# Kernel tuning notes

Measured on AMD Instinct MI355X. Metric: run time of the kernel, lower is better.

Reference implementation:

```python
import jax, jax.numpy as jnp
import numpy as np

TEMPERATURE = 0.07
BASE_TEMPERATURE = 0.07
N_CLASSES = 100


def setup_inputs() -> dict:
    key = jax.random.key(0)
    k1, k2, k3 = jax.random.split(key, 3)
    B, V, D = 4096, 2, 512
    features = jax.random.normal(k1, (B, V, D), dtype=jnp.float32)
    labels = jax.random.randint(k2, (B,), 0, N_CLASSES, dtype=jnp.int64)
    global_protos = jax.random.normal(k3, (N_CLASSES, D), dtype=jnp.float32)
    return {"features": features, "labels": labels, "global_protos": global_protos}


def reference(features, labels, global_protos):
    B, V, D = features.shape
    # contrast_feature = cat(unbind(features, dim=1)) -> view-major ordering [V*B, D]
    contrast = jnp.transpose(features, (1, 0, 2)).reshape(V * B, D)
    # anchor rows are prototypes gathered by label, tiled over views (contrast_mode='all')
    anchor = jnp.tile(global_protos[labels], (V, 1))          # [V*B, D]
    logits = (anchor @ contrast.T) / TEMPERATURE              # [V*B, V*B]
    logits = logits - jax.lax.stop_gradient(jnp.max(logits, axis=1, keepdims=True))
    # positive mask from label equality, tiled; diagonal (self-contrast) removed
    pos = (labels[:, None] == labels[None, :]).astype(jnp.float32)  # [B, B]
    mask = jnp.tile(pos, (V, V))                               # [V*B, V*B]
    logits_mask = 1.0 - jnp.eye(V * B, dtype=jnp.float32)
    mask = mask * logits_mask
    exp_logits = jnp.exp(logits) * logits_mask
    log_prob = logits - jnp.log(jnp.sum(exp_logits, axis=1, keepdims=True))
    mean_log_prob_pos = jnp.sum(mask * log_prob, axis=1) / jnp.sum(mask, axis=1)
    loss = -(TEMPERATURE / BASE_TEMPERATURE) * mean_log_prob_pos
    return jnp.mean(loss.reshape(V, B))
```

## Files before the change

kernel.cpp:

```cpp
#include <hip/hip_runtime.h>
#include <hip/hip_bf16.h>
#include <math.h>

#define BS 4096
#define DD 512
#define NCLS 100
#define NROWS 8192
#define NSLAB 256
#define INV_T (1.0f / 0.07f)

typedef __attribute__((ext_vector_type(8))) short short8;
typedef __attribute__((ext_vector_type(4))) float f32x4;

__device__ __forceinline__ unsigned short f2bf(float x) {
    __hip_bfloat16 h = __float2bfloat16(x);
    return *reinterpret_cast<unsigned short*>(&h);
}

__global__ __launch_bounds__(512) void k_gemm(const float* __restrict__ feats,
                                              const float* __restrict__ protos,
                                              const int* __restrict__ labels,
                                              float4* __restrict__ PA,
                                              float4* __restrict__ PB,
                                              float* __restrict__ stash,
                                              float* __restrict__ out) {
    __shared__ char lds[32 * DD * 2];
    const int nt = blockIdx.x, tid = threadIdx.x;
    if (nt == 0 && tid == 0) out[0] = 0.f;
    const int v  = nt >> 7;
    const int b0 = (nt & 127) * 32;

    float4 fr[8];
#pragma unroll
    for (int it = 0; it < 8; ++it) {
        const int i = tid + it * 512;
        const int r = i >> 7, c4 = i & 127;
        fr[it] = *(const float4*)(feats + (size_t)((b0 + r) * 2 + v) * DD + c4 * 4);
    }
#pragma unroll
    for (int it = 0; it < 8; ++it) {
        const int i = tid + it * 512;
        const int r = i >> 7, c4 = i & 127;
        ushort4 o = { f2bf(fr[it].x), f2bf(fr[it].y), f2bf(fr[it].z), f2bf(fr[it].w) };
        const int byte = (r * 1024 + c4 * 8) ^ ((r & 7) << 4);
        *reinterpret_cast<ushort4*>(&lds[byte]) = o;
    }
    __syncthreads();

    const int w = tid >> 6, lane = tid & 63;
    const int m = lane & 15, kb = lane >> 4;
    const int arow = min(w * 16 + m, NCLS - 1);
    const float4* ap = (const float4*)(protos + (size_t)arow * DD + kb * 8);

    const int swz   = (m & 7) << 4;
    const int base0 = m * 1024 + kb * 16;
    const int base1 = (m + 16) * 1024 + kb * 16;
    f32x4 acc0 = {}, acc1 = {};
#pragma unroll
    for (int k = 0; k < 16; ++k) {
        const float4 lo = ap[k * 8];
        const float4 hi = ap[k * 8 + 1];
        short8 a;
        a[0]=f2bf(lo.x); a[1]=f2bf(lo.y); a[2]=f2bf(lo.z); a[3]=f2bf(lo.w);
        a[4]=f2bf(hi.x); a[5]=f2bf(hi.y); a[6]=f2bf(hi.z); a[7]=f2bf(hi.w);
        const short8 bf0 = *reinterpret_cast<const short8*>(&lds[(base0 + k * 64) ^ swz]);
        const short8 bf1 = *reinterpret_cast<const short8*>(&lds[(base1 + k * 64) ^ swz]);
        acc0 = __builtin_amdgcn_mfma_f32_16x16x32_bf16(a, bf0, acc0, 0, 0, 0);
        acc1 = __builtin_amdgcn_mfma_f32_16x16x32_bf16(a, bf1, acc1, 0, 0, 0);
    }
#pragma unroll
    for (int r = 0; r < 4; ++r) { acc0[r] *= INV_T; acc1[r] *= INV_T; }

    const int j0 = nt * 32 + m, j1 = j0 + 16;
    const int lb0 = labels[j0 & (BS - 1)], lb1 = labels[j1 & (BS - 1)];

    if ((lb0 >> 4) == w && ((lb0 >> 2) & 3) == kb) {
        const int rr = lb0 & 3;
        stash[j0] = (rr==0)?acc0[0]:(rr==1)?acc0[1]:(rr==2)?acc0[2]:acc0[3];
    }
    if ((lb1 >> 4) == w && ((lb1 >> 2) & 3) == kb) {
        const int rr = lb1 & 3;
        stash[j1] = (rr==0)?acc1[0]:(rr==1)?acc1[1]:(rr==2)?acc1[2]:acc1[3];
    }

#pragma unroll
    for (int r = 0; r < 4; ++r) {
        const int row = w * 16 + kb * 4 + r;
        const float x0 = acc0[r], x1 = acc1[r];
        float m1, m2; int i1;
        if (x0 >= x1) { m1 = x0; m2 = x1; i1 = j0; } else { m1 = x1; m2 = x0; i1 = j1; }
#pragma unroll
        for (int s = 1; s < 16; s <<= 1) {
            const float om1 = __shfl_xor(m1, s);
            const float om2 = __shfl_xor(m2, s);
            const int   oi1 = __shfl_xor(i1, s);
            if (om1 > m1) { m2 = fmaxf(m1, om2); m1 = om1; i1 = oi1; }
            else          { m2 = fmaxf(m2, om1); }
        }
        float ea = __expf(x0 - m1) + __expf(x1 - m1);
        float ee = (j0 != i1 ? __expf(x0 - m2) : 0.f) + (j1 != i1 ? __expf(x1 - m2) : 0.f);
        float pp = 0.f, nn = 0.f;
        if (lb0 == row) { pp += x0 - m1; nn += 1.f; }
        if (lb1 == row) { pp += x1 - m1; nn += 1.f; }
#pragma unroll
        for (int s = 1; s < 16; s <<= 1) {
            ea += __shfl_xor(ea, s);
            ee += __shfl_xor(ee, s);
            pp += __shfl_xor(pp, s);
            nn += __shfl_xor(nn, s);
        }
        if (m == 0 && row < NCLS) {
            PA[row * NSLAB + nt] = make_float4(m1, m2, ea, ee);
            PB[row * NSLAB + nt] = make_float4(pp, nn, (float)i1, 0.f);
        }
    }
}

__global__ __launch_bounds__(256) void k_merge(const float4* __restrict__ PA,
                                               const float4* __restrict__ PB,
                                               const float* __restrict__ stash,
                                               const int* __restrict__ labels,
                                               float* __restrict__ out) {
    const int c = blockIdx.x, tid = threadIdx.x;
    const float4 A  = PA[c * NSLAB + tid];
    const float4 Bq = PB[c * NSLAB + tid];
    const float m1 = A.x, m2 = A.y, ea = A.z, ee = A.w;
    const float pp = Bq.x, nn = Bq.y;
    const int   i1 = (int)Bq.z;

    __shared__ float s1[256], s2[256];
    __shared__ int   si[256];
    s1[tid] = m1; s2[tid] = m2; si[tid] = i1;
    __syncthreads();
    for (int s = 128; s > 0; s >>= 1) {
        if (tid < s) {
            const float b1 = s1[tid + s], b2 = s2[tid + s];
            if (b1 > s1[tid]) { s2[tid] = fmaxf(s1[tid], b2); s1[tid] = b1; si[tid] = si[tid + s]; }
            else              { s2[tid] = fmaxf(s2[tid], b1); }
        }
        __syncthreads();
    }
    const float gm1 = s1[0], gm2 = s2[0];
    const int   gi1 = si[0];
    __syncthreads();

    const float e1c = ea * __expf(m1 - gm1);
    const float e2c = ((gi1 >> 5) == tid) ? ee * __expf(m2 - gm2)
                                          : ea * __expf(m1 - gm2);
    const float pc  = pp + nn * (m1 - gm1);
    __shared__ float r1[256], r2[256], r3[256];
    r1[tid] = e1c; r2[tid] = e2c; r3[tid] = pc;
    __syncthreads();
    for (int s = 128; s > 0; s >>= 1) {
        if (tid < s) { r1[tid] += r1[tid + s]; r2[tid] += r2[tid + s]; r3[tid] += r3[tid + s]; }
        __syncthreads();
    }
    const float E1 = r1[0], E2 = r2[0], Pg = r3[0];
    __syncthreads();

    float ls = 0.f;
    const float tmax = (gm2 - gm1) + __logf(E2);
    for (int it = 0; it < 8; ++it) {
        const int j = it * 1024 + tid * 4;
        const int4   lv = *(const int4*)(labels + (j & (BS - 1)));
        const float4 sv = *(const float4*)(stash + j);
        if (lv.x == c) ls += (j + 0 == gi1) ? tmax : __logf(E1 - __expf(sv.x - gm1));
        if (lv.y == c) ls += (j + 1 == gi1) ? tmax : __logf(E1 - __expf(sv.y - gm1));
        if (lv.z == c) ls += (j + 2 == gi1) ? tmax : __logf(E1 - __expf(sv.z - gm1));
        if (lv.w == c) ls += (j + 3 == gi1) ? tmax : __logf(E1 - __expf(sv.w - gm1));
    }
    s1[tid] = ls;
    __syncthreads();
    for (int s = 128; s > 0; s >>= 1) {
        if (tid < s) s1[tid] += s1[tid + s];
        __syncthreads();
    }
    if (tid == 0) atomicAdd(out, (s1[0] - Pg) / (float)NROWS);
}

extern "C" void kernel_launch(void* const* d_in, const int* in_sizes, int n_in,
                              void* d_out, int out_size, void* d_ws, size_t ws_size,
                              hipStream_t stream) {
    const float* feats  = (const float*)d_in[0];
    const int*   labels = (const int*)d_in[1];
    const float* protos = (const float*)d_in[2];
    float* out = (float*)d_out;

    char* w = (char*)d_ws;
    size_t off = 0;
    auto take = [&](size_t n) { size_t o = off; off += (n + 255) & ~(size_t)255; return o; };
    float4* PA    = (float4*)(w + take((size_t)NCLS * NSLAB * 16));
    float4* PB    = (float4*)(w + take((size_t)NCLS * NSLAB * 16));
    float*  stash = (float*)(w + take((size_t)NROWS * 4));

    k_gemm<<<NSLAB, 512, 0, stream>>>(feats, protos, labels, PA, PB, stash, out);
    k_merge<<<NCLS, 256, 0, stream>>>(PA, PB, stash, labels, out);
}
```

Before: 83.80 us.

## Pre-convert prototypes to bf16 and halve per-block column tile to 16

Adds a prep kernel that converts the 100 prototype rows to bf16 once into workspace and zeroes the output. The GEMM kernel then loads bf16 A fragments directly instead of converting fp32 per block. Each block now covers 16 contrast columns instead of 32, so there are 512 blocks for more parallelism across CUs. The merge kernel widens to 512 threads to reduce the larger partial set. This costs an extra kernel launch and doubles the partial-statistics traffic.

Result: no change. 84.19 us (+0.5%).

```diff
diff --git a/kernel.cpp b/kernel.cpp
--- a/kernel.cpp
+++ b/kernel.cpp
@@ -6,10 +6,11 @@
 #define DD 512
 #define NCLS 100
 #define NROWS 8192
-#define NSLAB 256
+#define NSLAB 512
 #define INV_T (1.0f / 0.07f)
 
 typedef __attribute__((ext_vector_type(8))) short short8;
+typedef __attribute__((ext_vector_type(8))) unsigned short ushort8;
 typedef __attribute__((ext_vector_type(4))) float f32x4;
 
 __device__ __forceinline__ unsigned short f2bf(float x) {
@@ -17,28 +18,49 @@
     return *reinterpret_cast<unsigned short*>(&h);
 }
 
+__global__ __launch_bounds__(256) void k_prep(const float* __restrict__ protos,
+                                              unsigned short* __restrict__ pB,
+                                              float* __restrict__ out) {
+    const int bid = blockIdx.x, tid = threadIdx.x;
+    if (bid < 28) {
+        const int t = bid * 256 + tid;
+        const int r = t >> 6;
+        const int kk = (t & 63) << 3;
+        float4 f0 = {0,0,0,0}, f1 = {0,0,0,0};
+        if (r < NCLS) {
+            const float4* s = (const float4*)(protos + (size_t)r * DD + kk);
+            f0 = s[0]; f1 = s[1];
+        }
+        ushort8 o;
+        o[0]=f2bf(f0.x); o[1]=f2bf(f0.y); o[2]=f2bf(f0.z); o[3]=f2bf(f0.w);
+        o[4]=f2bf(f1.x); o[5]=f2bf(f1.y); o[6]=f2bf(f1.z); o[7]=f2bf(f1.w);
+        *reinterpret_cast<ushort8*>(pB + (size_t)r * DD + kk) = o;
+    } else if (tid == 0) {
+        out[0] = 0.f;
+    }
+}
+
 __global__ __launch_bounds__(512) void k_gemm(const float* __restrict__ feats,
-                                              const float* __restrict__ protos,
+                                              const unsigned short* __restrict__ pB,
                                               const int* __restrict__ labels,
                                               float4* __restrict__ PA,
-                                              float4* __restrict__ PB,
-                                              float* __restrict__ stash,
-                                              float* __restrict__ out) {
-    __shared__ char lds[32 * DD * 2];
+                                              float4* __restrict__ PBd,
+                                              float* __restrict__ stash)
+{
+    __shared__ char lds[16 * DD * 2];
     const int nt = blockIdx.x, tid = threadIdx.x;
-    if (nt == 0 && tid == 0) out[0] = 0.f;
-    const int v  = nt >> 7;
-    const int b0 = (nt & 127) * 32;
-
-    float4 fr[8];
-#pragma unroll
-    for (int it = 0; it < 8; ++it) {
+    const int v  = nt >> 8;
+    const int b0 = (nt & 255) * 16;
+
+    float4 fr[4];
+#pragma unroll
+    for (int it = 0; it < 4; ++it) {
         const int i = tid + it * 512;
         const int r = i >> 7, c4 = i & 127;
         fr[it] = *(const float4*)(feats + (size_t)((b0 + r) * 2 + v) * DD + c4 * 4);
     }
 #pragma unroll
-    for (int it = 0; it < 8; ++it) {
+    for (int it = 0; it < 4; ++it) {
         const int i = tid + it * 512;
         const int r = i >> 7, c4 = i & 127;
         ushort4 o = { f2bf(fr[it].x), f2bf(fr[it].y), f2bf(fr[it].z), f2bf(fr[it].w) };
@@ -50,45 +72,33 @@
     const int w = tid >> 6, lane = tid & 63;
     const int m = lane & 15, kb = lane >> 4;
     const int arow = min(w * 16 + m, NCLS - 1);
-    const float4* ap = (const float4*)(protos + (size_t)arow * DD + kb * 8);
-
-    const int swz   = (m & 7) << 4;
-    const int base0 = m * 1024 + kb * 16;
-    const int base1 = (m + 16) * 1024 + kb * 16;
-    f32x4 acc0 = {}, acc1 = {};
+    const short8* apv = (const short8*)((const short*)pB + (size_t)arow * DD + kb * 8);
+
+    const int swz  = (m & 7) << 4;
+    const int base = m * 1024 + kb * 16;
+    f32x4 acc = {};
 #pragma unroll
     for (int k = 0; k < 16; ++k) {
-        const float4 lo = ap[k * 8];
-        const float4 hi = ap[k * 8 + 1];
-        short8 a;
-        a[0]=f2bf(lo.x); a[1]=f2bf(lo.y); a[2]=f2bf(lo.z); a[3]=f2bf(lo.w);
-        a[4]=f2bf(hi.x); a[5]=f2bf(hi.y); a[6]=f2bf(hi.z); a[7]=f2bf(hi.w);
-        const short8 bf0 = *reinterpret_cast<const short8*>(&lds[(base0 + k * 64) ^ swz]);
-        const short8 bf1 = *reinterpret_cast<const short8*>(&lds[(base1 + k * 64) ^ swz]);
-        acc0 = __builtin_amdgcn_mfma_f32_16x16x32_bf16(a, bf0, acc0, 0, 0, 0);
-        acc1 = __builtin_amdgcn_mfma_f32_16x16x32_bf16(a, bf1, acc1, 0, 0, 0);
-    }
-#pragma unroll
-    for (int r = 0; r < 4; ++r) { acc0[r] *= INV_T; acc1[r] *= INV_T; }
-
-    const int j0 = nt * 32 + m, j1 = j0 + 16;
-    const int lb0 = labels[j0 & (BS - 1)], lb1 = labels[j1 & (BS - 1)];
+        const short8 a = apv[k * 4];
+        const short8 b = *reinterpret_cast<const short8*>(&lds[(base + k * 64) ^ swz]);
+        acc = __builtin_amdgcn_mfma_f32_16x16x32_bf16(a, b, acc, 0, 0, 0);
+    }
+#pragma unroll
+    for (int r = 0; r < 4; ++r) acc[r] *= INV_T;
+
+    const int j0  = nt * 16 + m;
+    const int lb0 = labels[j0 & (BS - 1)];
 
     if ((lb0 >> 4) == w && ((lb0 >> 2) & 3) == kb) {
         const int rr = lb0 & 3;
-        stash[j0] = (rr==0)?acc0[0]:(rr==1)?acc0[1]:(rr==2)?acc0[2]:acc0[3];
-    }
-    if ((lb1 >> 4) == w && ((lb1 >> 2) & 3) == kb) {
-        const int rr = lb1 & 3;
-        stash[j1] = (rr==0)?acc1[0]:(rr==1)?acc1[1]:(rr==2)?acc1[2]:acc1[3];
+        stash[j0] = (rr==0)?acc[0]:(rr==1)?acc[1]:(rr==2)?acc[2]:acc[3];
     }
 
 #pragma unroll
     for (int r = 0; r < 4; ++r) {
         const int row = w * 16 + kb * 4 + r;
-        const float x0 = acc0[r], x1 = acc1[r];
-        float m1, m2; int i1;
-        if (x0 >= x1) { m1 = x0; m2 = x1; i1 = j0; } else { m1 = x1; m2 = x0; i1 = j1; }
+        const float x0 = acc[r];
+        float m1 = x0, m2 = -INFINITY; int i1 = j0;
 #pragma unroll
         for (int s = 1; s < 16; s <<= 1) {
             const float om1 = __shfl_xor(m1, s);
@@ -97,11 +107,10 @@
             if (om1 > m1) { m2 = fmaxf(m1, om2); m1 = om1; i1 = oi1; }
             else          { m2 = fmaxf(m2, om1); }
         }
-        float ea = __expf(x0 - m1) + __expf(x1 - m1);
-        float ee = (j0 != i1 ? __expf(x0 - m2) : 0.f) + (j1 != i1 ? __expf(x1 - m2) : 0.f);
-        float pp = 0.f, nn = 0.f;
-        if (lb0 == row) { pp += x0 - m1; nn += 1.f; }
-        if (lb1 == row) { pp += x1 - m1; nn += 1.f; }
+        float ea = __expf(x0 - m1);
+        float ee = (j0 != i1) ? __expf(x0 - m2) : 0.f;
+        float pp = (lb0 == row) ? x0 - m1 : 0.f;
+        float nn = (lb0 == row) ? 1.f : 0.f;
 #pragma unroll
         for (int s = 1; s < 16; s <<= 1) {
             ea += __shfl_xor(ea, s);
@@ -110,29 +119,29 @@
             nn += __shfl_xor(nn, s);
         }
         if (m == 0 && row < NCLS) {
-            PA[row * NSLAB + nt] = make_float4(m1, m2, ea, ee);
-            PB[row * NSLAB + nt] = make_float4(pp, nn, (float)i1, 0.f);
-        }
-    }
-}
-
-__global__ __launch_bounds__(256) void k_merge(const float4* __restrict__ PA,
-                                               const float4* __restrict__ PB,
+            PA[row * NSLAB + nt]  = make_float4(m1, m2, ea, ee);
+            PBd[row * NSLAB + nt] = make_float4(pp, nn, (float)i1, 0.f);
+        }
+    }
+}
+
+__global__ __launch_bounds__(512) void k_merge(const float4* __restrict__ PA,
+                                               const float4* __restrict__ PBd,
                                                const float* __restrict__ stash,
                                                const int* __restrict__ labels,
                                                float* __restrict__ out) {
     const int c = blockIdx.x, tid = threadIdx.x;
     const float4 A  = PA[c * NSLAB + tid];
-    const float4 Bq = PB[c * NSLAB + tid];
+    const float4 Bq = PBd[c * NSLAB + tid];
     const float m1 = A.x, m2 = A.y, ea = A.z, ee = A.w;
     const float pp = Bq.x, nn = Bq.y;
     const int   i1 = (int)Bq.z;
 
-    __shared__ float s1[256], s2[256];
-    __shared__ int   si[256];
+    __shared__ float s1[512], s2[512];
+    __shared__ int   si[512];
     s1[tid] = m1; s2[tid] = m2; si[tid] = i1;
     __syncthreads();
-    for (int s = 128; s > 0; s >>= 1) {
+    for (int s = 256; s > 0; s >>= 1) {
         if (tid < s) {
             const float b1 = s1[tid + s], b2 = s2[tid + s];
             if (b1 > s1[tid]) { s2[tid] = fmaxf(s1[tid], b2); s1[tid] = b1; si[tid] = si[tid + s]; }
@@ -145,13 +154,13 @@
     __syncthreads();
 
     const float e1c = ea * __expf(m1 - gm1);
-    const float e2c = ((gi1 >> 5) == tid) ? ee * __expf(m2 - gm2)
+    const float e2c = ((gi1 >> 4) == tid) ? ee * __expf(m2 - gm2)
                                           : ea * __expf(m1 - gm2);
     const float pc  = pp + nn * (m1 - gm1);
-    __shared__ float r1[256], r2[256], r3[256];
+    __shared__ float r1[512], r2[512], r3[512];
     r1[tid] = e1c; r2[tid] = e2c; r3[tid] = pc;
     __syncthreads();
-    for (int s = 128; s > 0; s >>= 1) {
+    for (int s = 256; s > 0; s >>= 1) {
         if (tid < s) { r1[tid] += r1[tid + s]; r2[tid] += r2[tid + s]; r3[tid] += r3[tid + s]; }
         __syncthreads();
     }
@@ -160,8 +169,8 @@
 
     float ls = 0.f;
     const float tmax = (gm2 - gm1) + __logf(E2);
-    for (int it = 0; it < 8; ++it) {
-        const int j = it * 1024 + tid * 4;
+    for (int it = 0; it < 4; ++it) {
+        const int j = it * 2048 + tid * 4;
         const int4   lv = *(const int4*)(labels + (j & (BS - 1)));
         const float4 sv = *(const float4*)(stash + j);
         if (lv.x == c) ls += (j + 0 == gi1) ? tmax : __logf(E1 - __expf(sv.x - gm1));
@@ -171,7 +180,7 @@
     }
     s1[tid] = ls;
     __syncthreads();
-    for (int s = 128; s > 0; s >>= 1) {
+    for (int s = 256; s > 0; s >>= 1) {
         if (tid < s) s1[tid] += s1[tid + s];
         __syncthreads();
     }
@@ -189,10 +198,12 @@
     char* w = (char*)d_ws;
     size_t off = 0;
     auto take = [&](size_t n) { size_t o = off; off += (n + 255) & ~(size_t)255; return o; };
-    float4* PA    = (float4*)(w + take((size_t)NCLS * NSLAB * 16));
-    float4* PB    = (float4*)(w + take((size_t)NCLS * NSLAB * 16));
-    float*  stash = (float*)(w + take((size_t)NROWS * 4));
-
-    k_gemm<<<NSLAB, 512, 0, stream>>>(feats, protos, labels, PA, PB, stash, out);
-    k_merge<<<NCLS, 256, 0, stream>>>(PA, PB, stash, labels, out);
-}
+    unsigned short* pB    = (unsigned short*)(w + take((size_t)112 * DD * 2));
+    float4*         PA    = (float4*)(w + take((size_t)NCLS * NSLAB * 16));
+    float4*         PBd   = (float4*)(w + take((size_t)NCLS * NSLAB * 16));
+    float*          stash = (float*)(w + take((size_t)NROWS * 4));
+
+    k_prep<<<29, 256, 0, stream>>>(protos, pB, out);
+    k_gemm<<<NSLAB, 512, 0, stream>>>(feats, pB, labels, PA, PBd, stash);
+    k_merge<<<NCLS, 512, 0, stream>>>(PA, PBd, stash, labels, out);
+}
```

## Fuse gemm and merge into one cooperative kernel with pre-converted bf16 prototypes

Applied to the files above, without the earlier changes.

Merges the two kernels into a single cooperative launch, using grid-wide syncs between stages so the second kernel launch gap disappears. Prototypes are converted to bf16 once into workspace instead of being re-converted from fp32 by every wave, which shrinks the A-operand loads. The merge stage now runs on 512 threads with padded reductions. The cost is two grid barriers, and a non-cooperative fallback path adds a third launch if the cooperative launch fails.

Measured after the change: 141.4 us. 1.69x slower.

```diff
diff --git a/kernel.cpp b/kernel.cpp
--- a/kernel.cpp
+++ b/kernel.cpp
@@ -1,6 +1,9 @@
 #include <hip/hip_runtime.h>
+#include <hip/hip_cooperative_groups.h>
 #include <hip/hip_bf16.h>
 #include <math.h>
+
+namespace cg = cooperative_groups;
 
 #define BS 4096
 #define DD 512
@@ -8,8 +11,10 @@
 #define NROWS 8192
 #define NSLAB 256
 #define INV_T (1.0f / 0.07f)
+#define NEG_BIG (-3.0e38f)
 
 typedef __attribute__((ext_vector_type(8))) short short8;
+typedef __attribute__((ext_vector_type(8))) unsigned short ushort8;
 typedef __attribute__((ext_vector_type(4))) float f32x4;
 
 __device__ __forceinline__ unsigned short f2bf(float x) {
@@ -17,19 +22,27 @@
     return *reinterpret_cast<unsigned short*>(&h);
 }
 
-__global__ __launch_bounds__(512) void k_gemm(const float* __restrict__ feats,
-                                              const float* __restrict__ protos,
-                                              const int* __restrict__ labels,
-                                              float4* __restrict__ PA,
-                                              float4* __restrict__ PB,
-                                              float* __restrict__ stash,
-                                              float* __restrict__ out) {
-    __shared__ char lds[32 * DD * 2];
-    const int nt = blockIdx.x, tid = threadIdx.x;
-    if (nt == 0 && tid == 0) out[0] = 0.f;
+__device__ __forceinline__ void conv_protos(int part, int tid,
+                                            const float* __restrict__ protos,
+                                            unsigned short* __restrict__ pB) {
+    const int t = part * 512 + tid;
+    const int r = t >> 6;
+    const int kk = (t & 63) << 3;
+    float4 f0 = {0,0,0,0}, f1 = {0,0,0,0};
+    if (r < NCLS) {
+        const float4* s = (const float4*)(protos + (size_t)r * DD + kk);
+        f0 = s[0]; f1 = s[1];
+    }
+    ushort8 o;
+    o[0]=f2bf(f0.x); o[1]=f2bf(f0.y); o[2]=f2bf(f0.z); o[3]=f2bf(f0.w);
+    o[4]=f2bf(f1.x); o[5]=f2bf(f1.y); o[6]=f2bf(f1.z); o[7]=f2bf(f1.w);
+    *reinterpret_cast<ushort8*>(pB + (size_t)r * DD + kk) = o;
+}
+
+__device__ __forceinline__ void gemm_stage(char* lds, int nt, int tid,
+                                           const float* __restrict__ feats) {
     const int v  = nt >> 7;
     const int b0 = (nt & 127) * 32;
-
     float4 fr[8];
 #pragma unroll
     for (int it = 0; it < 8; ++it) {
@@ -45,12 +58,19 @@
         const int byte = (r * 1024 + c4 * 8) ^ ((r & 7) << 4);
         *reinterpret_cast<ushort4*>(&lds[byte]) = o;
     }
-    __syncthreads();
-
+}
+
+__device__ __forceinline__ void gemm_main(char* lds, int nt, int tid,
+                                          const unsigned short* __restrict__ pB,
+                                          const int* __restrict__ labels,
+                                          float4* __restrict__ PA,
+                                          float4* __restrict__ PBd,
+                                          float* __restrict__ stash) {
+    __syncthreads();
     const int w = tid >> 6, lane = tid & 63;
     const int m = lane & 15, kb = lane >> 4;
     const int arow = min(w * 16 + m, NCLS - 1);
-    const float4* ap = (const float4*)(protos + (size_t)arow * DD + kb * 8);
+    const short8* apv = (const short8*)((const short*)pB + (size_t)arow * DD + kb * 8);
 
     const int swz   = (m & 7) << 4;
     const int base0 = m * 1024 + kb * 16;
@@ -58,11 +78,7 @@
     f32x4 acc0 = {}, acc1 = {};
 #pragma unroll
     for (int k = 0; k < 16; ++k) {
-        const float4 lo = ap[k * 8];
-        const float4 hi = ap[k * 8 + 1];
-        short8 a;
-        a[0]=f2bf(lo.x); a[1]=f2bf(lo.y); a[2]=f2bf(lo.z); a[3]=f2bf(lo.w);
-        a[4]=f2bf(hi.x); a[5]=f2bf(hi.y); a[6]=f2bf(hi.z); a[7]=f2bf(hi.w);
+        const short8 a   = apv[k * 4];
         const short8 bf0 = *reinterpret_cast<const short8*>(&lds[(base0 + k * 64) ^ swz]);
         const short8 bf1 = *reinterpret_cast<const short8*>(&lds[(base1 + k * 64) ^ swz]);
         acc0 = __builtin_amdgcn_mfma_f32_16x16x32_bf16(a, bf0, acc0, 0, 0, 0);
@@ -110,29 +126,37 @@
             nn += __shfl_xor(nn, s);
         }
         if (m == 0 && row < NCLS) {
-            PA[row * NSLAB + nt] = make_float4(m1, m2, ea, ee);
-            PB[row * NSLAB + nt] = make_float4(pp, nn, (float)i1, 0.f);
-        }
-    }
-}
-
-__global__ __launch_bounds__(256) void k_merge(const float4* __restrict__ PA,
-                                               const float4* __restrict__ PB,
-                                               const float* __restrict__ stash,
-                                               const int* __restrict__ labels,
-                                               float* __restrict__ out) {
-    const int c = blockIdx.x, tid = threadIdx.x;
-    const float4 A  = PA[c * NSLAB + tid];
-    const float4 Bq = PB[c * NSLAB + tid];
-    const float m1 = A.x, m2 = A.y, ea = A.z, ee = A.w;
-    const float pp = Bq.x, nn = Bq.y;
-    const int   i1 = (int)Bq.z;
-
-    __shared__ float s1[256], s2[256];
-    __shared__ int   si[256];
+            PA[row * NSLAB + nt]  = make_float4(m1, m2, ea, ee);
+            PBd[row * NSLAB + nt] = make_float4(pp, nn, (float)i1, 0.f);
+        }
+    }
+}
+
+__device__ __forceinline__ void merge_class(char* ldsraw, int c, int tid,
+                                            const float4* __restrict__ PA,
+                                            const float4* __restrict__ PBd,
+                                            const float* __restrict__ stash,
+                                            const int* __restrict__ labels,
+                                            float* __restrict__ out) {
+    float* s1 = (float*)ldsraw;
+    float* s2 = s1 + 512;
+    int*   si = (int*)(s2 + 512);
+    float* r1 = (float*)(si + 512);
+    float* r2 = r1 + 512;
+    float* r3 = r2 + 512;
+
+    float m1, m2, ea, ee, pp, nn; int i1;
+    if (tid < NSLAB) {
+        const float4 A  = PA[c * NSLAB + tid];
+        const float4 Bq = PBd[c * NSLAB + tid];
+        m1 = A.x; m2 = A.y; ea = A.z; ee = A.w;
+        pp = Bq.x; nn = Bq.y; i1 = (int)Bq.z;
+    } else {
+        m1 = NEG_BIG; m2 = NEG_BIG; ea = 0.f; ee = 0.f; pp = 0.f; nn = 0.f; i1 = -1;
+    }
     s1[tid] = m1; s2[tid] = m2; si[tid] = i1;
     __syncthreads();
-    for (int s = 128; s > 0; s >>= 1) {
+    for (int s = 256; s > 0; s >>= 1) {
         if (tid < s) {
             const float b1 = s1[tid + s], b2 = s2[tid + s];
             if (b1 > s1[tid]) { s2[tid] = fmaxf(s1[tid], b2); s1[tid] = b1; si[tid] = si[tid + s]; }
@@ -145,13 +169,12 @@
     __syncthreads();
 
     const float e1c = ea * __expf(m1 - gm1);
-    const float e2c = ((gi1 >> 5) == tid) ? ee * __expf(m2 - gm2)
-                                          : ea * __expf(m1 - gm2);
+    const float e2c = (tid < NSLAB && (gi1 >> 5) == tid) ? ee * __expf(m2 - gm2)
+                                                         : ea * __expf(m1 - gm2);
     const float pc  = pp + nn * (m1 - gm1);
-    __shared__ float r1[256], r2[256], r3[256];
     r1[tid] = e1c; r2[tid] = e2c; r3[tid] = pc;
     __syncthreads();
-    for (int s = 128; s > 0; s >>= 1) {
+    for (int s = 256; s > 0; s >>= 1) {
         if (tid < s) { r1[tid] += r1[tid + s]; r2[tid] += r2[tid + s]; r3[tid] += r3[tid + s]; }
         __syncthreads();
     }
@@ -160,8 +183,9 @@
 
     float ls = 0.f;
     const float tmax = (gm2 - gm1) + __logf(E2);
-    for (int it = 0; it < 8; ++it) {
-        const int j = it * 1024 + tid * 4;
+#pragma unroll
+    for (int it = 0; it < 4; ++it) {
+        const int j = it * 2048 + tid * 4;
         const int4   lv = *(const int4*)(labels + (j & (BS - 1)));
         const float4 sv = *(const float4*)(stash + j);
         if (lv.x == c) ls += (j + 0 == gi1) ? tmax : __logf(E1 - __expf(sv.x - gm1));
@@ -171,11 +195,60 @@
     }
     s1[tid] = ls;
     __syncthreads();
-    for (int s = 128; s > 0; s >>= 1) {
+    for (int s = 256; s > 0; s >>= 1) {
         if (tid < s) s1[tid] += s1[tid + s];
         __syncthreads();
     }
     if (tid == 0) atomicAdd(out, (s1[0] - Pg) / (float)NROWS);
+}
+
+__global__ __launch_bounds__(512) void k_fused(const float* __restrict__ feats,
+                                               const float* __restrict__ protos,
+                                               const int* __restrict__ labels,
+                                               unsigned short* __restrict__ pB,
+                                               float4* __restrict__ PA,
+                                               float4* __restrict__ PBd,
+                                               float* __restrict__ stash,
+                                               float* __restrict__ out) {
+    __shared__ char lds[32 * DD * 2];
+    const int nt = blockIdx.x, tid = threadIdx.x;
+
+    gemm_stage(lds, nt, tid, feats);
+    if (nt >= 128 && nt < 142) conv_protos(nt - 128, tid, protos, pB);
+    if (nt == 0 && tid == 0) out[0] = 0.f;
+    cg::this_grid().sync();
+
+    gemm_main(lds, nt, tid, pB, labels, PA, PBd, stash);
+    cg::this_grid().sync();
+
+    if (nt < NCLS) merge_class(lds, nt, tid, PA, PBd, stash, labels, out);
+}
+
+__global__ __launch_bounds__(512) void k_prep_fb(const float* __restrict__ protos,
+                                                 unsigned short* __restrict__ pB,
+                                                 float* __restrict__ out) {
+    if (blockIdx.x < 14) conv_protos(blockIdx.x, threadIdx.x, protos, pB);
+    else if (threadIdx.x == 0) out[0] = 0.f;
+}
+
+__global__ __launch_bounds__(512) void k_gemm_fb(const float* __restrict__ feats,
+                                                 const unsigned short* __restrict__ pB,
+                                                 const int* __restrict__ labels,
+                                                 float4* __restrict__ PA,
+                                                 float4* __restrict__ PBd,
+                                                 float* __restrict__ stash) {
+    __shared__ char lds[32 * DD * 2];
+    gemm_stage(lds, blockIdx.x, threadIdx.x, feats);
+    gemm_main(lds, blockIdx.x, threadIdx.x, pB, labels, PA, PBd, stash);
+}
+
+__global__ __launch_bounds__(512) void k_merge_fb(const float4* __restrict__ PA,
+                                                  const float4* __restrict__ PBd,
+                                                  const float* __restrict__ stash,
+                                                  const int* __restrict__ labels,
+                                                  float* __restrict__ out) {
+    __shared__ char lds[512 * 4 * 6];
+    merge_class(lds, blockIdx.x, threadIdx.x, PA, PBd, stash, labels, out);
 }
 
 extern "C" void kernel_launch(void* const* d_in, const int* in_sizes, int n_in,
@@ -189,10 +262,18 @@
     char* w = (char*)d_ws;
     size_t off = 0;
     auto take = [&](size_t n) { size_t o = off; off += (n + 255) & ~(size_t)255; return o; };
-    float4* PA    = (float4*)(w + take((size_t)NCLS * NSLAB * 16));
-    float4* PB    = (float4*)(w + take((size_t)NCLS * NSLAB * 16));
-    float*  stash = (float*)(w + take((size_t)NROWS * 4));
-
-    k_gemm<<<NSLAB, 512, 0, stream>>>(feats, protos, labels, PA, PB, stash, out);
-    k_merge<<<NCLS, 256, 0, stream>>>(PA, PB, stash, labels, out);
-}
+    unsigned short* pB    = (unsigned short*)(w + take((size_t)112 * DD * 2));
+    float4*         PA    = (float4*)(w + take((size_t)NCLS * NSLAB * 16));
+    float4*         PBd   = (float4*)(w + take((size_t)NCLS * NSLAB * 16));
+    float*          stash = (float*)(w + take((size_t)NROWS * 4));
+
+    void* args[] = { (void*)&feats, (void*)&protos, (void*)&labels, (void*)&pB,
+                     (void*)&PA, (void*)&PBd, (void*)&stash, (void*)&out };
+    hipError_t e = hipLaunchCooperativeKernel((const void*)k_fused, dim3(NSLAB), dim3(512),
+                                              args, 0, stream);
+    if (e != hipSuccess) {
+        k_prep_fb<<<15, 512, 0, stream>>>(protos, pB, out);
+        k_gemm_fb<<<NSLAB, 512, 0, stream>>>(feats, pB, labels, PA, PBd, stash);
+        k_merge_fb<<<NCLS, 512, 0, stream>>>(PA, PBd, stash, labels, out);
+    }
+}
```
